# Optimization experiments

Measured on AMD Instinct MI355X. Metric: run time of the kernel, lower is better.

The kernel has to match this reference:

```python
import jax, jax.numpy as jnp
import numpy as np
from jax import lax

G, N, S, K, R = 8, 4096, 2048, 64, 0.4   # graphs, nodes/graph, fps samples (ratio=0.5), max neighbors, radius
EPER = 65536                              # edges per graph (avg degree 16)
C = 13                                    # num_classes


def setup_inputs():
    key = jax.random.key(0)
    ks = jax.random.split(key, 8)
    norm = jax.random.normal(ks[0], (G * N, 3), jnp.float32)
    pos = jax.random.uniform(ks[1], (G * N, 3), jnp.float32)
    x = jax.random.normal(ks[2], (G * N, 2), jnp.float32)
    e = jax.random.randint(ks[3], (2, G, EPER), 0, N)
    off = (jnp.arange(G) * N)[None, :, None]
    edge_index = (e + off).reshape(2, G * EPER).astype(jnp.int64)
    batch = jnp.repeat(jnp.arange(G), N).astype(jnp.int64)
    def lin(k, i, o):
        return jax.random.normal(k, (i, o), jnp.float32) / np.float32(np.sqrt(i))
    W1 = lin(ks[4], 8, 64);    b1 = jnp.zeros((64,), jnp.float32)
    W2 = lin(ks[5], 72, 128);  b2 = jnp.zeros((128,), jnp.float32)
    W3 = lin(ks[6], 139, 256); b3 = jnp.zeros((256,), jnp.float32)
    lin_w = lin(ks[7], 256, C); lin_b = jnp.zeros((C,), jnp.float32)
    return dict(norm=norm, pos=pos, x=x, edge_index=edge_index, batch=batch,
                W1=W1, b1=b1, W2=W2, b2=b2, W3=W3, b3=b3, lin_w=lin_w, lin_b=lin_b)


def _gcn(h, src, dst, ew, W, b, n):
    # GCNConv(normalize=False): out[dst] += ew * (h @ W)[src]; + bias
    m = (h @ W)[src] * ew[:, None]
    return jax.ops.segment_sum(m, dst, num_segments=n) + b


def _fps(p):  # farthest point sampling on one graph, p: [N,3] -> [S] local indices (start at node 0)
    def step(carry, _):
        mind, cur = carry
        d = jnp.sum((p - p[cur]) ** 2, axis=1)
        mind = jnp.minimum(mind, d)
        return (mind, jnp.argmax(mind).astype(jnp.int32)), cur
    _, idx = lax.scan(step, (jnp.full((N,), jnp.inf, p.dtype), jnp.int32(0)), None, length=S)
    return idx


def _radius(p, q):  # p [N,3], q [S,3] -> neighbor cols [S,K] (lowest-index-first within radius), valid mask
    d2 = jnp.sum((q[:, None, :] - p[None, :, :]) ** 2, axis=-1)  # [S,N]
    mask = d2 < R * R
    score = jnp.where(mask, N - jnp.arange(N, dtype=jnp.int32)[None, :], 0)
    vals, cols = lax.top_k(score, K)
    valid = vals > 0
    return jnp.where(valid, cols, 0), valid


def reference(norm, pos, x, edge_index, batch, W1, b1, W2, b2, W3, b3, lin_w, lin_b):
    NT = G * N
    inp = jnp.concatenate([norm, pos, x], axis=1)          # [NT, 8]
    src, dst = edge_index[0], edge_index[1]
    ew = jnp.ones((src.shape[0],), inp.dtype)
    # dropout is inactive at inference (training=False)
    h1 = jax.nn.relu(_gcn(inp, src, dst, ew, W1, b1, NT))  # [NT, 64]
    h1 = jnp.concatenate([h1, inp], axis=1)                # [NT, 72]
    h2 = jax.nn.relu(_gcn(h1, src, dst, ew, W2, b2, NT))   # [NT, 128]

    pg = pos.reshape(G, N, 3)
    pgs = lax.stop_gradient(pg)
    idx_loc = jax.vmap(_fps)(pgs)                          # [G, S] local indices
    q = jax.vmap(lambda p, i: p[i])(pg, idx_loc)           # [G, S, 3] sampled positions
    cols, valid = jax.vmap(_radius)(pgs, lax.stop_gradient(q))  # [G, S, K]

    # PointConv with identity local_nn/global_nn: max over neighbors of [x_j, pos_j - pos_i]
    hg = h2.reshape(G, N, 128)
    def pconv(h, p, qv, c, v):
        msg = jnp.concatenate([h[c], p[c] - qv[:, None, :]], axis=-1)  # [S, K, 131]
        msg = jnp.where(v[..., None], msg, -jnp.inf)
        return jnp.max(msg, axis=1)                                    # [S, 131]
    x_int = jax.vmap(pconv)(hg, pg, q, cols, valid).reshape(G * S, 131)

    # filter_adj: keep edges with both endpoints sampled, remap to new ids
    idx_flat = (idx_loc + (jnp.arange(G) * N)[:, None]).reshape(-1)    # [G*S] global indices
    mapping = jnp.full((NT,), -1, jnp.int32).at[idx_flat].set(jnp.arange(G * S, dtype=jnp.int32))
    ns, nd = mapping[src], mapping[dst]
    em = (ns >= 0) & (nd >= 0)
    ew3 = em.astype(inp.dtype)
    ns = jnp.where(em, ns, 0)
    nd = jnp.where(em, nd, 0)

    h3in = jnp.concatenate([x_int, inp[idx_flat]], axis=1)  # [G*S, 139]
    h3 = jax.nn.relu(_gcn(h3in, ns, nd, ew3, W3, b3, G * S))  # [G*S, 256]

    pooled = h3.reshape(G, S, 256).max(axis=1)              # global_max_pool -> [G, 256]
    logits = pooled @ lin_w + lin_b
    out = jax.nn.log_softmax(logits, axis=1)
    pred = jax.nn.softmax(out, axis=1)
    return (out, pred)
```

## Files before the change

### kernel.cpp

```cpp
#include <hip/hip_runtime.h>
#include <hip/hip_bf16.h>

constexpr int NG   = 8;
constexpr int NPG  = 4096;
constexpr int NT   = NG * NPG;
constexpr int NS   = 2048;
constexpr int GS   = NG * NS;
constexpr int KN   = 64;
constexpr int NE   = NG * 65536;
constexpr int NC   = 13;
constexpr int NWORK = 248;
constexpr int SPB  = 16;
constexpr int NF3B = GS / SPB;

__device__ __forceinline__ float inp_val(const float* norm, const float* pos, const float* x,
                                         int node, int dim) {
  if (dim < 3) return norm[(size_t)node * 3 + dim];
  if (dim < 6) return pos[(size_t)node * 3 + (dim - 3)];
  return x[(size_t)node * 2 + (dim - 6)];
}

__device__ __forceinline__ void wbar(int* ctrs, int k, int target) {
  __syncthreads();
  __threadfence();
  if (threadIdx.x == 0) {
    __hip_atomic_fetch_add(&ctrs[k], 1, __ATOMIC_RELEASE, __HIP_MEMORY_SCOPE_AGENT);
    while (__hip_atomic_load(&ctrs[k], __ATOMIC_ACQUIRE, __HIP_MEMORY_SCOPE_AGENT) < target)
      __builtin_amdgcn_s_sleep(16);
  }
  __syncthreads();
}

__global__ __launch_bounds__(256, 1) void phaseA_kernel(
    const float* __restrict__ pos, int* __restrict__ idxf, float* __restrict__ qpos,
    const float* __restrict__ norm, const float* __restrict__ x,
    const float* __restrict__ W1, float* __restrict__ t1,
    const int* __restrict__ ei, int* __restrict__ deg,
    int* __restrict__ off1, int* __restrict__ cur1, int* __restrict__ el1,
    const float* __restrict__ b1, const float* __restrict__ W2, float* __restrict__ t2,
    const float* __restrict__ b2, float* __restrict__ h2,
    int* __restrict__ wctr) {
  if (blockIdx.x >= 8) {
    const int wb = blockIdx.x - 8;
    const int sub = threadIdx.x >> 6;
    const int f = threadIdx.x & 63;
    __shared__ float wrow[4][80];
    __shared__ int sscan[256];
    for (int n0 = wb * 4; n0 < NT; n0 += NWORK * 4) {
      int n = n0 + sub;
      if (f < 8) wrow[sub][f] = inp_val(norm, pos, x, n, f);
      float acc = 0.f;
#pragma unroll
      for (int i = 0; i < 8; ++i) acc += wrow[sub][i] * W1[i * 64 + f];
      t1[(size_t)n * 64 + f] = acc;
    }
    for (int e = wb * 256 + threadIdx.x; e < NE; e += NWORK * 256)
      atomicAdd(&deg[ei[NE + e]], 1);
    wbar(wctr, 0, NWORK);
    if (wb == 0) {
      int t = threadIdx.x, base = t * 128, s = 0;
      for (int i = 0; i < 128; ++i) s += deg[base + i];
      sscan[t] = s;
      __syncthreads();
      for (int d = 1; d < 256; d <<= 1) {
        int v = (t >= d) ? sscan[t - d] : 0;
        __syncthreads();
        sscan[t] += v;
        __syncthreads();
      }
      int excl = (t == 0) ? 0 : sscan[t - 1];
      for (int i = 0; i < 128; ++i) { off1[base + i] = excl; excl += deg[base + i]; }
      if (t == 255) off1[NT] = sscan[255];
    }
    wbar(wctr, 1, NWORK);
    for (int e = wb * 256 + threadIdx.x; e < NE; e += NWORK * 256) {
      int sN = ei[e], dN = ei[NE + e];
      int p = off1[dN] + atomicAdd(&cur1[dN], 1);
      el1[p] = sN;
    }
    wbar(wctr, 2, NWORK);
    for (int n0 = wb * 4; n0 < NT; n0 += NWORK * 4) {
      int n = n0 + sub;
      int e0 = off1[n], e1 = off1[n + 1];
      float acc = 0.f;
      for (int j = e0; j < e1; ++j) acc += t1[(size_t)el1[j] * 64 + f];
      wrow[sub][f] = fmaxf(acc + b1[f], 0.f);
      if (f < 8) wrow[sub][64 + f] = inp_val(norm, pos, x, n, f);
      float a0 = 0.f, a1 = 0.f;
#pragma unroll 8
      for (int i = 0; i < 72; ++i) {
        float r = wrow[sub][i];
        a0 += r * W2[i * 128 + f];
        a1 += r * W2[i * 128 + 64 + f];
      }
      t2[(size_t)n * 128 + f] = a0;
      t2[(size_t)n * 128 + 64 + f] = a1;
    }
    wbar(wctr, 3, NWORK);
    {
      const int f2 = threadIdx.x & 127, sub2 = threadIdx.x >> 7;
      for (int n0 = wb * 2; n0 < NT; n0 += NWORK * 2) {
        int n = n0 + sub2;
        int e0 = off1[n], e1 = off1[n + 1];
        float acc = 0.f;
        for (int j = e0; j < e1; ++j) acc += t2[(size_t)el1[j] * 128 + f2];
        h2[(size_t)n * 128 + f2] = fmaxf(acc + b2[f2], 0.f);
      }
    }
    return;
  }
  const int g = blockIdx.x;
  __shared__ float4 sq[2][4];
  __shared__ int sidx[2][4];
  __shared__ float4 qrec[NS];
  __shared__ int irec[NS];
  const float* pg = pos + (size_t)g * NPG * 3;
  const int tid = threadIdx.x;
  const int wave = tid >> 6, lane = tid & 63;
  const int p0 = tid * 16;

  float a[48];
  {
    const float4* pg4 = reinterpret_cast<const float4*>(pg + (size_t)p0 * 3);
#pragma unroll
    for (int j = 0; j < 12; ++j) {
      float4 t = pg4[j];
      a[4 * j + 0] = t.x; a[4 * j + 1] = t.y; a[4 * j + 2] = t.z; a[4 * j + 3] = t.w;
    }
  }
  float px[16], py[16], pz[16], mind[16];
#pragma unroll
  for (int i = 0; i < 16; ++i) {
    px[i] = a[3 * i]; py[i] = a[3 * i + 1]; pz[i] = a[3 * i + 2];
    mind[i] = __int_as_float(0x7f800000);
  }
  float cx = pg[0], cy = pg[1], cz = pg[2];
  int idx_sel = 0;

  for (int s = 0; s < NS; ++s) {
    if (tid == 0) { irec[s] = idx_sel; qrec[s] = make_float4(cx, cy, cz, 0.f); }
    float bestv = -1.f, bx = 0.f, by = 0.f, bz = 0.f;
    int bi = 0;
#pragma unroll
    for (int i = 0; i < 16; ++i) {
      float dx = __fsub_rn(px[i], cx);
      float dy = __fsub_rn(py[i], cy);
      float dz = __fsub_rn(pz[i], cz);
      float dd = __fadd_rn(__fadd_rn(__fmul_rn(dx, dx), __fmul_rn(dy, dy)), __fmul_rn(dz, dz));
      float nm = fminf(mind[i], dd);
      mind[i] = nm;
      bool gt = nm > bestv;
      bestv = gt ? nm : bestv;
      bx = gt ? px[i] : bx;
      by = gt ? py[i] : by;
      bz = gt ? pz[i] : bz;
      bi = gt ? i : bi;
    }
    float v = bestv;
    v = fmaxf(v, __int_as_float(__builtin_amdgcn_update_dpp(0, __float_as_int(v), 0x111, 0xF, 0xF, true)));
    v = fmaxf(v, __int_as_float(__builtin_amdgcn_update_dpp(0, __float_as_int(v), 0x112, 0xF, 0xF, true)));
    v = fmaxf(v, __int_as_float(__builtin_amdgcn_update_dpp(0, __float_as_int(v), 0x114, 0xF, 0xF, true)));
    v = fmaxf(v, __int_as_float(__builtin_amdgcn_update_dpp(0, __float_as_int(v), 0x118, 0xF, 0xF, true)));
    v = fmaxf(v, __int_as_float(__builtin_amdgcn_update_dpp(0, __float_as_int(v), 0x142, 0xF, 0xF, true)));
    v = fmaxf(v, __int_as_float(__builtin_amdgcn_update_dpp(0, __float_as_int(v), 0x143, 0xF, 0xF, true)));
    int maxbits = __builtin_amdgcn_readlane(__float_as_int(v), 63);
    float wavemax = __int_as_float(maxbits);
    unsigned long long ball = __ballot(bestv == wavemax);
    int winner = __ffsll(ball) - 1;
    int b = s & 1;
    if (lane == winner) {
      sq[b][wave] = make_float4(bx, by, bz, wavemax);
      sidx[b][wave] = p0 + bi;
    }
    __syncthreads();
    float4 q0 = sq[b][0], q1 = sq[b][1], q2 = sq[b][2], q3 = sq[b][3];
    float4 qs = q3;
    if (q2.w >= qs.w) qs = q2;
    if (q1.w >= qs.w) qs = q1;
    if (q0.w >= qs.w) qs = q0;
    cx = qs.x; cy = qs.y; cz = qs.z;
    if (tid == 0) {
      int i0 = sidx[b][0], i1 = sidx[b][1], i2 = sidx[b][2], i3 = sidx[b][3];
      float r = q3.w; int is = i3;
      if (q2.w >= r) { r = q2.w; is = i2; }
      if (q1.w >= r) { r = q1.w; is = i1; }
      if (q0.w >= r) { r = q0.w; is = i0; }
      idx_sel = is;
    }
  }
  __syncthreads();
  for (int j = tid; j < NS; j += 256) {
    idxf[g * NS + j] = g * NPG + irec[j];
    float4 q = qrec[j];
    size_t m = (size_t)(g * NS + j) * 3;
    qpos[m + 0] = q.x; qpos[m + 1] = q.y; qpos[m + 2] = q.z;
  }
}

__global__ __launch_bounds__(256, 1) void radius_kernel(
    const float* __restrict__ pos, const float* __restrict__ qpos,
    int* __restrict__ cols, int* __restrict__ cnt,
    const int* __restrict__ idxf, int* __restrict__ mp) {
  __shared__ float spx[NPG], spy[NPG], spz[NPG];
  __shared__ int sbuf[KN][64][4];
  const int g = blockIdx.x & 7;
  const int s0 = (blockIdx.x >> 3) * 64;
  const float* pgc = pos + (size_t)g * NPG * 3;
  for (int i = threadIdx.x; i < NPG * 3; i += 256) {
    float v = pgc[i]; int node = i / 3, cc = i - node * 3;
    if (cc == 0) spx[node] = v; else if (cc == 1) spy[node] = v; else spz[node] = v;
  }
  __syncthreads();
  const int group = threadIdx.x >> 2;
  const int j = threadIdx.x & 3;
  const int m = g * NS + s0 + group;
  if (j == 0) mp[idxf[m]] = m;
  const float qx = qpos[(size_t)m * 3], qy = qpos[(size_t)m * 3 + 1],
              qz = qpos[(size_t)m * 3 + 2];
  int c = 0;
  const int i0 = j * 1024;
  for (int i = i0; i < i0 + 1024; ++i) {
    float dx = __fsub_rn(spx[i], qx);
    float dy = __fsub_rn(spy[i], qy);
    float dz = __fsub_rn(spz[i], qz);
    float d2 = __fadd_rn(__fadd_rn(__fmul_rn(dx, dx), __fmul_rn(dy, dy)), __fmul_rn(dz, dz));
    if (d2 < 0.16f) {
      sbuf[c][group][j] = i;
      if (++c == KN) break;
    }
  }
  const int lbase = (threadIdx.x & 63) & ~3;
  int c0 = __shfl(c, lbase + 0), c1 = __shfl(c, lbase + 1),
      c2 = __shfl(c, lbase + 2), c3 = __shfl(c, lbase + 3);
  int pre = (j > 0 ? c0 : 0) + (j > 1 ? c1 : 0) + (j > 2 ? c2 : 0);
  int total = c0 + c1 + c2 + c3;
  if (j == 0) cnt[m] = total < KN ? total : KN;
  int take = KN - pre;
  take = take < 0 ? 0 : (take > c ? c : take);
  int* outp = cols + (size_t)m * KN + pre;
  for (int i = 0; i < take; ++i) outp[i] = sbuf[i][group][j];
}

__global__ __launch_bounds__(256) void pointconv_kernel(const float* __restrict__ h2,
                                                        const float* __restrict__ pos,
                                                        const float* __restrict__ qpos,
                                                        const int* __restrict__ cols,
                                                        const int* __restrict__ cnt,
                                                        float* __restrict__ xint) {
  const int g = blockIdx.x & 7;
  const int chunk = blockIdx.x >> 3;
  const int ss = threadIdx.x >> 6;
  const int t = threadIdx.x & 63;
  const int m = g * NS + chunk * 4 + ss;
  int n = cnt[m];
  const int* cl = cols + (size_t)m * KN;
  float m0 = -INFINITY, m1 = -INFINITY, mp = -INFINITY;
  for (int k = 0; k < n; ++k) {
    int c = cl[k];
    size_t base = (size_t)(g * NPG + c);
    m0 = fmaxf(m0, h2[base * 128 + t]);
    m1 = fmaxf(m1, h2[base * 128 + 64 + t]);
    if (t < 3) mp = fmaxf(mp, pos[base * 3 + t]);
  }
  float* xo = xint + (size_t)m * 131;
  xo[t] = m0;
  xo[64 + t] = m1;
  if (t < 3) xo[128 + t] = __fsub_rn(mp, qpos[(size_t)m * 3 + t]);
}

__global__ void post2_kernel(const float* __restrict__ xint, const int* __restrict__ idxf,
                             const float* __restrict__ norm, const float* __restrict__ pos,
                             const float* __restrict__ x, const float* __restrict__ W3,
                             float* __restrict__ t3,
                             const int* __restrict__ ei, const int* __restrict__ mp,
                             int* __restrict__ deg) {
  if (blockIdx.x >= NF3B) {
    int wb = blockIdx.x - NF3B;
    int eb = (wb & 7) * 256 + (wb >> 3);
    int e = eb * 256 + threadIdx.x;
    int ns = mp[ei[e]], nd = mp[ei[NE + e]];
    if (ns >= 0 && nd >= 0) atomicAdd(&deg[nd], 1);
    return;
  }
  __shared__ float srow[SPB][140];
  const int m0 = blockIdx.x * SPB;
  for (int jj = threadIdx.x; jj < SPB * 139; jj += 256) {
    int sub = jj / 139, i = jj - sub * 139;
    int m = m0 + sub;
    srow[sub][i] = (i < 131) ? xint[(size_t)m * 131 + i]
                             : inp_val(norm, pos, x, idxf[m], i - 131);
  }
  __syncthreads();
  int f = threadIdx.x;
  float acc[SPB];
#pragma unroll
  for (int s = 0; s < SPB; ++s) acc[s] = 0.f;
#pragma unroll 4
  for (int i = 0; i < 139; ++i) {
    float wv = W3[i * 256 + f];
#pragma unroll
    for (int s = 0; s < SPB; ++s) acc[s] += srow[s][i] * wv;
  }
#pragma unroll
  for (int s = 0; s < SPB; ++s) t3[(size_t)(m0 + s) * 256 + f] = acc[s];
}

__global__ void fill2_kernel(const int* __restrict__ ei, const int* __restrict__ mp,
                             const int* __restrict__ off, int* __restrict__ cur,
                             int* __restrict__ el) {
  int b = blockIdx.x;
  int eb = (b & 7) * 256 + (b >> 3);
  int e = eb * 256 + threadIdx.x;
  int ns = mp[ei[e]], nd = mp[ei[NE + e]];
  if (ns >= 0 && nd >= 0) {
    int p = off[nd] + atomicAdd(&cur[nd], 1);
    el[p] = ns;
  }
}

__global__ __launch_bounds__(1024) void scan_kernel(const int* __restrict__ in,
                                                    int* __restrict__ out, int n) {
  __shared__ int ls[1024];
  int tid = threadIdx.x;
  int per = (n + 1023) >> 10;
  int base = tid * per;
  int s = 0;
  for (int i = 0; i < per; ++i) { int idx = base + i; if (idx < n) s += in[idx]; }
  ls[tid] = s;
  __syncthreads();
  for (int d = 1; d < 1024; d <<= 1) {
    int v = (tid >= d) ? ls[tid - d] : 0;
    __syncthreads();
    ls[tid] += v;
    __syncthreads();
  }
  int excl = (tid == 0) ? 0 : ls[tid - 1];
  for (int i = 0; i < per; ++i) {
    int idx = base + i;
    if (idx < n) { out[idx] = excl; excl += in[idx]; }
  }
  if (tid == 1023) out[n] = ls[1023];
}

__global__ void aggpool_kernel(const float* __restrict__ t, const int* __restrict__ off,
                               const int* __restrict__ el, const float* __restrict__ b,
                               float* __restrict__ pooled) {
  int node = (blockIdx.x & 7) * 2048 + (blockIdx.x >> 3);
  int f = threadIdx.x;
  int e0 = off[node], e1 = off[node + 1];
  float acc = 0.f;
  for (int j = e0; j < e1; ++j) acc += t[(size_t)el[j] * 256 + f];
  float val = fmaxf(acc + b[f], 0.f);
  atomicMax((int*)pooled + (node >> 11) * 256 + f, __float_as_int(val));
}

__global__ void head_kernel(const float* __restrict__ pooled, const float* __restrict__ lw,
                            const float* __restrict__ lb, float* __restrict__ outp) {
  __shared__ float lg[NG * NC];
  int t = threadIdx.x;
  if (t < NG * NC) {
    int g = t / NC, c = t % NC;
    float acc = lb[c];
    for (int k = 0; k < 256; ++k) acc += pooled[g * 256 + k] * lw[k * NC + c];
    lg[t] = acc;
  }
  __syncthreads();
  if (t < NG) {
    int g = t;
    float mx = -INFINITY;
    for (int c = 0; c < NC; ++c) mx = fmaxf(mx, lg[g * NC + c]);
    float sum = 0.f;
    for (int c = 0; c < NC; ++c) sum += expf(lg[g * NC + c] - mx);
    float lse = logf(sum);
    float ov[NC];
    float mx2 = -INFINITY;
    for (int c = 0; c < NC; ++c) {
      ov[c] = lg[g * NC + c] - mx - lse;
      outp[g * NC + c] = ov[c];
      mx2 = fmaxf(mx2, ov[c]);
    }
    float s2 = 0.f;
    for (int c = 0; c < NC; ++c) s2 += expf(ov[c] - mx2);
    for (int c = 0; c < NC; ++c) outp[NG * NC + g * NC + c] = expf(ov[c] - mx2) / s2;
  }
}

extern "C" void kernel_launch(void* const* d_in, const int* in_sizes, int n_in,
                              void* d_out, int out_size, void* d_ws, size_t ws_size,
                              hipStream_t stream) {
  const float* norm = (const float*)d_in[0];
  const float* pos  = (const float*)d_in[1];
  const float* x    = (const float*)d_in[2];
  const int* ei     = (const int*)d_in[3];
  const float* W1 = (const float*)d_in[5];
  const float* b1 = (const float*)d_in[6];
  const float* W2 = (const float*)d_in[7];
  const float* b2 = (const float*)d_in[8];
  const float* W3 = (const float*)d_in[9];
  const float* b3 = (const float*)d_in[10];
  const float* lw = (const float*)d_in[11];
  const float* lb = (const float*)d_in[12];
  float* outp = (float*)d_out;

  char* w = (char*)d_ws;
  size_t o = 0;
  auto alloc = [&](size_t bytes) -> void* {
    void* p = w + o;
    o = (o + bytes + 255) & ~(size_t)255;
    return p;
  };
  int* deg1   = (int*)alloc((size_t)NT * 4);
  int* cur1   = (int*)alloc((size_t)NT * 4);
  int* deg2   = (int*)alloc((size_t)GS * 4);
  int* cur2   = (int*)alloc((size_t)GS * 4);
  float* pooled = (float*)alloc((size_t)NG * 256 * 4);
  int* wctr   = (int*)alloc(128);
  size_t zlen = o;
  float* A    = (float*)alloc((size_t)NT * 128 * 4);
  float* Bf   = (float*)alloc((size_t)NT * 128 * 4);
  float* T1   = (float*)alloc((size_t)NT * 64 * 4);
  float* xint = (float*)alloc((size_t)GS * 131 * 4);
  int* cols   = (int*)alloc((size_t)GS * KN * 4);
  int* cnt    = (int*)alloc((size_t)GS * 4);
  int* off1   = (int*)alloc((size_t)(NT + 1) * 4);
  int* el1    = (int*)alloc((size_t)NE * 4);
  int* off2   = (int*)alloc((size_t)(GS + 1) * 4);
  int* el2    = (int*)alloc((size_t)NE * 4);
  int* idxf   = (int*)alloc((size_t)GS * 4);
  float* qpos = (float*)alloc((size_t)GS * 3 * 4);
  int* mapv   = (int*)alloc((size_t)NT * 4);

  hipMemsetAsync(w, 0, zlen, stream);
  hipMemsetAsync(mapv, 0xFF, (size_t)NT * 4, stream);

  {
    void* ka[] = {(void*)&pos, (void*)&idxf, (void*)&qpos, (void*)&norm, (void*)&x,
                  (void*)&W1, (void*)&T1, (void*)&ei, (void*)&deg1,
                  (void*)&off1, (void*)&cur1, (void*)&el1,
                  (void*)&b1, (void*)&W2, (void*)&A, (void*)&b2, (void*)&Bf,
                  (void*)&wctr};
    hipLaunchCooperativeKernel((const void*)phaseA_kernel, dim3(8 + NWORK), dim3(256),
                               ka, 0, stream);
  }
  radius_kernel<<<256, 256, 0, stream>>>(pos, qpos, cols, cnt, idxf, mapv);
  pointconv_kernel<<<GS / 4, 256, 0, stream>>>(Bf, pos, qpos, cols, cnt, xint);
  post2_kernel<<<NF3B + 2048, 256, 0, stream>>>(xint, idxf, norm, pos, x, W3, A,
                                                ei, mapv, deg2);
  scan_kernel<<<1, 1024, 0, stream>>>(deg2, off2, GS);
  fill2_kernel<<<2048, 256, 0, stream>>>(ei, mapv, off2, cur2, el2);
  aggpool_kernel<<<GS, 256, 0, stream>>>(A, off2, el2, b3, pooled);
  head_kernel<<<1, 128, 0, stream>>>(pooled, lw, lb, outp);
}
```

Before: 1.987 ms.

## Fuse radius search and point conv into cooperative kernel, streaming FPS samples

Moves the radius neighbor search and the point-conv max aggregation into the worker blocks of the cooperative phase A kernel. The FPS blocks now publish sample positions and indices every 64 steps behind a release counter. Worker blocks grab 256-sample chunks from an atomic queue and wait until those samples exist, so neighbor search overlaps the serial FPS loop and two kernel launches disappear. In exchange, each thread scans up to 4096 points serially (where four threads previously shared one query), shared memory per block grows, and spin-waiting blocks may contend with FPS.

```diff
diff --git a/kernel.cpp b/kernel.cpp
--- a/kernel.cpp
+++ b/kernel.cpp
@@ -10,6 +10,7 @@
 constexpr int NE   = NG * 65536;
 constexpr int NC   = 13;
 constexpr int NWORK = 248;
+constexpr int NSTR = 64;
 constexpr int SPB  = 16;
 constexpr int NF3B = GS / SPB;
 
@@ -39,13 +40,17 @@
     int* __restrict__ off1, int* __restrict__ cur1, int* __restrict__ el1,
     const float* __restrict__ b1, const float* __restrict__ W2, float* __restrict__ t2,
     const float* __restrict__ b2, float* __restrict__ h2,
-    int* __restrict__ wctr) {
+    int* __restrict__ mapv, int* __restrict__ cols, int* __restrict__ cnt,
+    float* __restrict__ xint, int* __restrict__ wctr) {
   if (blockIdx.x >= 8) {
     const int wb = blockIdx.x - 8;
     const int sub = threadIdx.x >> 6;
     const int f = threadIdx.x & 63;
     __shared__ float wrow[4][80];
     __shared__ int sscan[256];
+    __shared__ float spx[NPG], spy[NPG], spz[NPG];
+    __shared__ int scnt[256];
+    __shared__ int schunk;
     for (int n0 = wb * 4; n0 < NT; n0 += NWORK * 4) {
       int n = n0 + sub;
       if (f < 8) wrow[sub][f] = inp_val(norm, pos, x, n, f);
@@ -106,6 +111,69 @@
         for (int j = e0; j < e1; ++j) acc += t2[(size_t)el1[j] * 128 + f2];
         h2[(size_t)n * 128 + f2] = fmaxf(acc + b2[f2], 0.f);
       }
+    }
+    if (wb >= NSTR) return;
+    for (;;) {
+      if (threadIdx.x == 0)
+        schunk = __hip_atomic_fetch_add(&wctr[8], 1, __ATOMIC_RELAXED,
+                                        __HIP_MEMORY_SCOPE_AGENT);
+      __syncthreads();
+      int chunk = schunk;
+      __syncthreads();
+      if (chunk >= 64) break;
+      int gC = chunk >> 3, c0 = (chunk & 7) * 256;
+      const float* pgc = pos + (size_t)gC * NPG * 3;
+      for (int i = threadIdx.x; i < NPG * 3; i += 256) {
+        float v = pgc[i]; int node = i / 3, cc = i - node * 3;
+        if (cc == 0) spx[node] = v; else if (cc == 1) spy[node] = v; else spz[node] = v;
+      }
+      if (threadIdx.x == 0) {
+        while (__hip_atomic_load(&wctr[32 + gC * 32], __ATOMIC_ACQUIRE,
+                                 __HIP_MEMORY_SCOPE_AGENT) < c0 + 256)
+          __builtin_amdgcn_s_sleep(64);
+      }
+      __syncthreads();
+      {
+        int m = gC * NS + c0 + threadIdx.x;
+        mapv[idxf[m]] = m;
+        float qx = qpos[(size_t)m * 3], qy = qpos[(size_t)m * 3 + 1],
+              qz = qpos[(size_t)m * 3 + 2];
+        int* out = cols + (size_t)m * KN;
+        int c = 0;
+        for (int i = 0; i < NPG; ++i) {
+          float dx = __fsub_rn(spx[i], qx);
+          float dy = __fsub_rn(spy[i], qy);
+          float dz = __fsub_rn(spz[i], qz);
+          float d2 = __fadd_rn(__fadd_rn(__fmul_rn(dx, dx), __fmul_rn(dy, dy)),
+                               __fmul_rn(dz, dz));
+          if (d2 < 0.16f) {
+            out[c++] = i;
+            if (c == KN) break;
+          }
+        }
+        scnt[threadIdx.x] = c;
+        cnt[m] = c;
+      }
+      __syncthreads();
+      for (int ss = (threadIdx.x >> 6); ss < 256; ss += 4) {
+        int fc = threadIdx.x & 63;
+        int m = gC * NS + c0 + ss;
+        int n = scnt[ss];
+        const int* cl = cols + (size_t)m * KN;
+        float m0 = -INFINITY, m1 = -INFINITY, mpv = -INFINITY;
+        for (int k = 0; k < n; ++k) {
+          int cc = cl[k];
+          size_t b = (size_t)(gC * NPG + cc);
+          m0 = fmaxf(m0, h2[b * 128 + fc]);
+          m1 = fmaxf(m1, h2[b * 128 + 64 + fc]);
+          if (fc < 3) mpv = fmaxf(mpv, (fc == 0 ? spx[cc] : (fc == 1 ? spy[cc] : spz[cc])));
+        }
+        float* xo = xint + (size_t)m * 131;
+        xo[fc] = m0;
+        xo[64 + fc] = m1;
+        if (fc < 3) xo[128 + fc] = __fsub_rn(mpv, qpos[(size_t)m * 3 + fc]);
+      }
+      __syncthreads();
     }
     return;
   }
@@ -187,85 +255,18 @@
       if (q0.w >= r) { r = q0.w; is = i0; }
       idx_sel = is;
     }
-  }
-  __syncthreads();
-  for (int j = tid; j < NS; j += 256) {
-    idxf[g * NS + j] = g * NPG + irec[j];
-    float4 q = qrec[j];
-    size_t m = (size_t)(g * NS + j) * 3;
-    qpos[m + 0] = q.x; qpos[m + 1] = q.y; qpos[m + 2] = q.z;
-  }
-}
-
-__global__ __launch_bounds__(256, 1) void radius_kernel(
-    const float* __restrict__ pos, const float* __restrict__ qpos,
-    int* __restrict__ cols, int* __restrict__ cnt,
-    const int* __restrict__ idxf, int* __restrict__ mp) {
-  __shared__ float spx[NPG], spy[NPG], spz[NPG];
-  __shared__ int sbuf[KN][64][4];
-  const int g = blockIdx.x & 7;
-  const int s0 = (blockIdx.x >> 3) * 64;
-  const float* pgc = pos + (size_t)g * NPG * 3;
-  for (int i = threadIdx.x; i < NPG * 3; i += 256) {
-    float v = pgc[i]; int node = i / 3, cc = i - node * 3;
-    if (cc == 0) spx[node] = v; else if (cc == 1) spy[node] = v; else spz[node] = v;
-  }
-  __syncthreads();
-  const int group = threadIdx.x >> 2;
-  const int j = threadIdx.x & 3;
-  const int m = g * NS + s0 + group;
-  if (j == 0) mp[idxf[m]] = m;
-  const float qx = qpos[(size_t)m * 3], qy = qpos[(size_t)m * 3 + 1],
-              qz = qpos[(size_t)m * 3 + 2];
-  int c = 0;
-  const int i0 = j * 1024;
-  for (int i = i0; i < i0 + 1024; ++i) {
-    float dx = __fsub_rn(spx[i], qx);
-    float dy = __fsub_rn(spy[i], qy);
-    float dz = __fsub_rn(spz[i], qz);
-    float d2 = __fadd_rn(__fadd_rn(__fmul_rn(dx, dx), __fmul_rn(dy, dy)), __fmul_rn(dz, dz));
-    if (d2 < 0.16f) {
-      sbuf[c][group][j] = i;
-      if (++c == KN) break;
-    }
-  }
-  const int lbase = (threadIdx.x & 63) & ~3;
-  int c0 = __shfl(c, lbase + 0), c1 = __shfl(c, lbase + 1),
-      c2 = __shfl(c, lbase + 2), c3 = __shfl(c, lbase + 3);
-  int pre = (j > 0 ? c0 : 0) + (j > 1 ? c1 : 0) + (j > 2 ? c2 : 0);
-  int total = c0 + c1 + c2 + c3;
-  if (j == 0) cnt[m] = total < KN ? total : KN;
-  int take = KN - pre;
-  take = take < 0 ? 0 : (take > c ? c : take);
-  int* outp = cols + (size_t)m * KN + pre;
-  for (int i = 0; i < take; ++i) outp[i] = sbuf[i][group][j];
-}
-
-__global__ __launch_bounds__(256) void pointconv_kernel(const float* __restrict__ h2,
-                                                        const float* __restrict__ pos,
-                                                        const float* __restrict__ qpos,
-                                                        const int* __restrict__ cols,
-                                                        const int* __restrict__ cnt,
-                                                        float* __restrict__ xint) {
-  const int g = blockIdx.x & 7;
-  const int chunk = blockIdx.x >> 3;
-  const int ss = threadIdx.x >> 6;
-  const int t = threadIdx.x & 63;
-  const int m = g * NS + chunk * 4 + ss;
-  int n = cnt[m];
-  const int* cl = cols + (size_t)m * KN;
-  float m0 = -INFINITY, m1 = -INFINITY, mp = -INFINITY;
-  for (int k = 0; k < n; ++k) {
-    int c = cl[k];
-    size_t base = (size_t)(g * NPG + c);
-    m0 = fmaxf(m0, h2[base * 128 + t]);
-    m1 = fmaxf(m1, h2[base * 128 + 64 + t]);
-    if (t < 3) mp = fmaxf(mp, pos[base * 3 + t]);
-  }
-  float* xo = xint + (size_t)m * 131;
-  xo[t] = m0;
-  xo[64 + t] = m1;
-  if (t < 3) xo[128 + t] = __fsub_rn(mp, qpos[(size_t)m * 3 + t]);
+    if ((s & 63) == 63) {
+      int smp = (s - 63) + (tid >> 2);
+      int comp = tid & 3;
+      if (comp < 3) qpos[(size_t)(g * NS + smp) * 3 + comp] = ((float*)&qrec[smp])[comp];
+      else idxf[g * NS + smp] = g * NPG + irec[smp];
+      __threadfence();
+      __syncthreads();
+      if (tid == 0)
+        __hip_atomic_store(&wctr[32 + g * 32], s + 1, __ATOMIC_RELEASE,
+                           __HIP_MEMORY_SCOPE_AGENT);
+    }
+  }
 }
 
 __global__ void post2_kernel(const float* __restrict__ xint, const int* __restrict__ idxf,
@@ -414,7 +415,7 @@
   int* deg2   = (int*)alloc((size_t)GS * 4);
   int* cur2   = (int*)alloc((size_t)GS * 4);
   float* pooled = (float*)alloc((size_t)NG * 256 * 4);
-  int* wctr   = (int*)alloc(128);
+  int* wctr   = (int*)alloc(2048);
   size_t zlen = o;
   float* A    = (float*)alloc((size_t)NT * 128 * 4);
   float* Bf   = (float*)alloc((size_t)NT * 128 * 4);
@@ -438,12 +439,11 @@
                   (void*)&W1, (void*)&T1, (void*)&ei, (void*)&deg1,
                   (void*)&off1, (void*)&cur1, (void*)&el1,
                   (void*)&b1, (void*)&W2, (void*)&A, (void*)&b2, (void*)&Bf,
+                  (void*)&mapv, (void*)&cols, (void*)&cnt, (void*)&xint,
                   (void*)&wctr};
     hipLaunchCooperativeKernel((const void*)phaseA_kernel, dim3(8 + NWORK), dim3(256),
                                ka, 0, stream);
   }
-  radius_kernel<<<256, 256, 0, stream>>>(pos, qpos, cols, cnt, idxf, mapv);
-  pointconv_kernel<<<GS / 4, 256, 0, stream>>>(Bf, pos, qpos, cols, cnt, xint);
   post2_kernel<<<NF3B + 2048, 256, 0, stream>>>(xint, idxf, norm, pos, x, W3, A,
                                                 ei, mapv, deg2);
   scan_kernel<<<1, 1024, 0, stream>>>(deg2, off2, GS);
```

Result: slower. 3.007 ms (+51.4%).
